# Optimization experiments

Measured on AMD Instinct MI355X. Metric: run time of the kernel, lower is better.

Reference implementation:

```python
import jax, jax.numpy as jnp
import numpy as np

NBITS = 4
GROUP_SIZE = 128


def setup_inputs() -> dict:
    key = jax.random.key(0)
    k1, k2, k3, k4, k5 = jax.random.split(key, 5)
    B, S, K, N = 2, 2048, 4096, 4096
    G = K // GROUP_SIZE  # 32 groups along K
    x = jax.random.normal(k1, (B, S, K), dtype=jnp.float16)
    # unpacked uint4 weights stored in int32 carrier, values in [0, 2^nbits)
    W_q = jax.random.randint(k2, (N, K), 0, 2 ** NBITS, dtype=jnp.int32)
    scale = (jax.random.uniform(k3, (N, G), dtype=jnp.float32) * 0.01 + 0.001).astype(jnp.float16)
    zero = (jax.random.uniform(k4, (N, G), dtype=jnp.float32) * (2 ** NBITS)).astype(jnp.float16)
    bias = jax.random.normal(k5, (N,), dtype=jnp.float16)
    return {"x": x, "W_q": W_q, "scale": scale, "zero": zero, "bias": bias}


def _dequant(W_q, scale, zero):
    # W_q: [N, K] int, scale/zero: [N, K//group_size] fp16
    # zeros_mode='original': W = (W_q - zero) * scale, per group along K
    N, K = W_q.shape
    G = K // GROUP_SIZE
    Wg = W_q.reshape(N, G, GROUP_SIZE).astype(jnp.float16)
    Wd = (Wg - zero[:, :, None]) * scale[:, :, None]
    return Wd.reshape(N, K)


def reference(x, W_q, scale, zero, bias):
    # out = x @ W_deq^T + bias   (layout 'nt': W is [N, K])
    W = _dequant(W_q, scale, zero)            # [N, K] fp16
    out = jnp.einsum('bsk,nk->bsn', x, W)     # [B, S, N] fp16 accum per module config
    return out + bias
```

## Files before the change

kernel.cpp:

```cpp
#include <hip/hip_runtime.h>
#include <hip/hip_bf16.h>


typedef __bf16 bf16x8 __attribute__((ext_vector_type(8)));
typedef float f32x4 __attribute__((ext_vector_type(4)));

#define BM 128
#define BN 128
#define BK 64

static __device__ __forceinline__ int pack_bf16x2(float a, float b) {
    __hip_bfloat162 p = __float22bfloat162_rn(make_float2(a, b));
    int r;
    __builtin_memcpy(&r, &p, 4);
    return r;
}

__global__ __launch_bounds__(256) void prepass_kernel(
    const float* __restrict__ X, unsigned short* __restrict__ Ad,
    const int*   __restrict__ Wq,
    const float* __restrict__ scale,
    const float* __restrict__ zero,
    unsigned short* __restrict__ Wd,
    int aUnits, int wUnits, int K, int G, int GROUP)
{
    const int stride = gridDim.x * blockDim.x;
    const int t0     = blockIdx.x * blockDim.x + threadIdx.x;

    for (int u = t0; u < aUnits; u += stride) {
        const long long f = (long long)u * 8;
        const float4 a0 = *(const float4*)(X + f);
        const float4 a1 = *(const float4*)(X + f + 4);
        int4 d;
        d.x = pack_bf16x2(a0.x, a0.y);
        d.y = pack_bf16x2(a0.z, a0.w);
        d.z = pack_bf16x2(a1.x, a1.y);
        d.w = pack_bf16x2(a1.z, a1.w);
        *(int4*)(Ad + f) = d;
    }

    const int unitsPerRow = K >> 3;
    for (int u = t0; u < wUnits; u += stride) {
        const int n = u / unitsPerRow;
        const int k = (u - n * unitsPerRow) * 8;
        const int g = k / GROUP;
        const float s  = scale[(long long)n * G + g];
        const float z  = zero [(long long)n * G + g];
        const float mz = -z * s;

        const long long f = (long long)n * K + k;
        const int4 q0 = *(const int4*)(Wq + f);
        const int4 q1 = *(const int4*)(Wq + f + 4);
        int4 d;
        d.x = pack_bf16x2((float)q0.x * s + mz, (float)q0.y * s + mz);
        d.y = pack_bf16x2((float)q0.z * s + mz, (float)q0.w * s + mz);
        d.z = pack_bf16x2((float)q1.x * s + mz, (float)q1.y * s + mz);
        d.w = pack_bf16x2((float)q1.z * s + mz, (float)q1.w * s + mz);
        *(int4*)(Wd + f) = d;
    }
}

__global__ __launch_bounds__(256, 2) void gemm_bf16_nt(
    const unsigned short* __restrict__ A,
    const unsigned short* __restrict__ Bw,
    const float* __restrict__ bias,
    float*       __restrict__ C,
    int M, int N, int K)
{
    __shared__ unsigned short ldsA[BM * BK];
    __shared__ unsigned short ldsB[BN * BK];

    const int tid   = threadIdx.x;
    const int lane  = tid & 63;
    const int wave  = tid >> 6;
    const int waveM = wave >> 1;
    const int waveN = wave & 1;

    const int blockN0 = blockIdx.x * BN;
    const int blockM0 = blockIdx.y * BM;

    const long long aBase = (long long)blockM0 * K;
    const long long bBase = (long long)blockN0 * K;

    const int rowInChunk = lane >> 3;
    const int colChunkSw = (lane & 7) ^ rowInChunk;
    const int col8       = colChunkSw * 8;

    f32x4 acc[4][4];
#pragma unroll
    for (int i = 0; i < 4; ++i)
#pragma unroll
        for (int j = 0; j < 4; ++j)
            acc[i][j] = (f32x4){0.f, 0.f, 0.f, 0.f};

    const int row16 = lane & 15;
    const int quad  = lane >> 4;
    const int sw    = row16 & 7;

    for (int k0 = 0; k0 < K; k0 += BK) {
        __syncthreads();
#pragma unroll
        for (int c = 0; c < 4; ++c) {
            const int chunk = (wave << 2) | c;
            const int row   = (chunk << 3) | rowInChunk;
            const unsigned short* gA = A  + aBase + (long long)row * K + k0 + col8;
            const unsigned short* gB = Bw + bBase + (long long)row * K + k0 + col8;
            __builtin_amdgcn_global_load_lds(
                (const __attribute__((address_space(1))) unsigned int*)gA,
                (__attribute__((address_space(3))) unsigned int*)&ldsA[chunk * 512],
                16, 0, 0);
            __builtin_amdgcn_global_load_lds(
                (const __attribute__((address_space(1))) unsigned int*)gB,
                (__attribute__((address_space(3))) unsigned int*)&ldsB[chunk * 512],
                16, 0, 0);
        }
        __syncthreads();

#pragma unroll
        for (int kk = 0; kk < 2; ++kk) {
            bf16x8 av[4], bv[4];
#pragma unroll
            for (int i = 0; i < 4; ++i) {
                const int r    = waveM * 64 + i * 16 + row16;
                const int slot = (kk * 4 + quad) ^ sw;
                av[i] = *(const bf16x8*)&ldsA[r * BK + slot * 8];
            }
#pragma unroll
            for (int j = 0; j < 4; ++j) {
                const int r    = waveN * 64 + j * 16 + row16;
                const int slot = (kk * 4 + quad) ^ sw;
                bv[j] = *(const bf16x8*)&ldsB[r * BK + slot * 8];
            }
#pragma unroll
            for (int i = 0; i < 4; ++i)
#pragma unroll
                for (int j = 0; j < 4; ++j)
                    acc[i][j] = __builtin_amdgcn_mfma_f32_16x16x32_bf16(
                        av[i], bv[j], acc[i][j], 0, 0, 0);
        }
    }

    const int colBase = blockN0 + waveN * 64;
    const int rowBase = blockM0 + waveM * 64;
    float biasf[4];
#pragma unroll
    for (int j = 0; j < 4; ++j)
        biasf[j] = bias[colBase + j * 16 + row16];

#pragma unroll
    for (int i = 0; i < 4; ++i) {
        const int row0 = rowBase + i * 16 + quad * 4;
#pragma unroll
        for (int j = 0; j < 4; ++j) {
            const int col = colBase + j * 16 + row16;
#pragma unroll
            for (int r = 0; r < 4; ++r) {
                C[(long long)(row0 + r) * N + col] = acc[i][j][r] + biasf[j];
            }
        }
    }
}

__global__ __launch_bounds__(256) void hqq_gemm_fused_f32(
    const float* __restrict__ A,
    const int*   __restrict__ Wq,
    const float* __restrict__ scale,
    const float* __restrict__ zero,
    const float* __restrict__ bias,
    float*       __restrict__ C,
    int M, int N, int K, int G, int GROUP)
{
    __shared__ unsigned short ldsA[BM * BK];
    __shared__ unsigned short ldsB[BN * BK];

    const int tid   = threadIdx.x;
    const int lane  = tid & 63;
    const int wave  = tid >> 6;
    const int waveM = wave >> 1;
    const int waveN = wave & 1;

    const int blockN0 = blockIdx.x * BN;
    const int blockM0 = blockIdx.y * BM;

    const int row16 = lane & 15;
    const int quad  = lane >> 4;

    f32x4 acc[4][4];
#pragma unroll
    for (int i = 0; i < 4; ++i)
#pragma unroll
        for (int j = 0; j < 4; ++j)
            acc[i][j] = (f32x4){0.f, 0.f, 0.f, 0.f};

    for (int k0 = 0; k0 < K; k0 += BK) {
        const int g = k0 / GROUP;
        int4 ra[4], rb[4];
#pragma unroll
        for (int c = 0; c < 4; ++c) {
            const int chunk = c * 256 + tid;
            const int row   = chunk >> 3;
            const int col   = (chunk & 7) * 8;

            const float* ap = A + (long long)(blockM0 + row) * K + k0 + col;
            const float4 a0 = *(const float4*)(ap);
            const float4 a1 = *(const float4*)(ap + 4);
            int4 da;
            da.x = pack_bf16x2(a0.x, a0.y);
            da.y = pack_bf16x2(a0.z, a0.w);
            da.z = pack_bf16x2(a1.x, a1.y);
            da.w = pack_bf16x2(a1.z, a1.w);
            ra[c] = da;

            const int n = blockN0 + row;
            const float s  = scale[(long long)n * G + g];
            const float z  = zero [(long long)n * G + g];
            const float mz = -z * s;
            const long long wb = (long long)n * K + k0 + col;
            const int4 q0 = *(const int4*)(Wq + wb);
            const int4 q1 = *(const int4*)(Wq + wb + 4);
            int4 db;
            db.x = pack_bf16x2((float)q0.x * s + mz, (float)q0.y * s + mz);
            db.y = pack_bf16x2((float)q0.z * s + mz, (float)q0.w * s + mz);
            db.z = pack_bf16x2((float)q1.x * s + mz, (float)q1.y * s + mz);
            db.w = pack_bf16x2((float)q1.z * s + mz, (float)q1.w * s + mz);
            rb[c] = db;
        }

        __syncthreads();
#pragma unroll
        for (int c = 0; c < 4; ++c) {
            const int chunk = c * 256 + tid;
            *(int4*)&ldsA[chunk * 8] = ra[c];
            *(int4*)&ldsB[chunk * 8] = rb[c];
        }
        __syncthreads();

#pragma unroll
        for (int kk = 0; kk < 2; ++kk) {
            const int kOff = kk * 32 + quad * 8;
            bf16x8 av[4], bv[4];
#pragma unroll
            for (int i = 0; i < 4; ++i)
                av[i] = *(const bf16x8*)&ldsA[(waveM * 64 + i * 16 + row16) * BK + kOff];
#pragma unroll
            for (int j = 0; j < 4; ++j)
                bv[j] = *(const bf16x8*)&ldsB[(waveN * 64 + j * 16 + row16) * BK + kOff];
#pragma unroll
            for (int i = 0; i < 4; ++i)
#pragma unroll
                for (int j = 0; j < 4; ++j)
                    acc[i][j] = __builtin_amdgcn_mfma_f32_16x16x32_bf16(
                        av[i], bv[j], acc[i][j], 0, 0, 0);
        }
    }

    const int colBase = blockN0 + waveN * 64;
    const int rowBase = blockM0 + waveM * 64;
    float biasf[4];
#pragma unroll
    for (int j = 0; j < 4; ++j)
        biasf[j] = bias[colBase + j * 16 + row16];

#pragma unroll
    for (int i = 0; i < 4; ++i) {
        const int row0 = rowBase + i * 16 + quad * 4;
#pragma unroll
        for (int j = 0; j < 4; ++j) {
            const int col = colBase + j * 16 + row16;
#pragma unroll
            for (int r = 0; r < 4; ++r) {
                C[(long long)(row0 + r) * N + col] = acc[i][j][r] + biasf[j];
            }
        }
    }
}

extern "C" void kernel_launch(void* const* d_in, const int* in_sizes, int n_in,
                              void* d_out, int out_size, void* d_ws, size_t ws_size,
                              hipStream_t stream) {
    (void)n_in; (void)out_size;

    const float* x     = (const float*)d_in[0];
    const int*   Wq    = (const int*)d_in[1];
    const float* scale = (const float*)d_in[2];
    const float* zero  = (const float*)d_in[3];
    const float* bias  = (const float*)d_in[4];
    float*       out   = (float*)d_out;

    const int N     = in_sizes[4];
    const int G     = in_sizes[2] / N;
    const int K     = in_sizes[1] / N;
    const int M     = in_sizes[0] / K;
    const int GROUP = K / G;

    const size_t needWs = (size_t)N * K * 2 + (size_t)M * K * 2;

    if (ws_size >= needWs) {
        unsigned short* Wd = (unsigned short*)d_ws;
        unsigned short* Ad = (unsigned short*)((char*)d_ws + (size_t)N * K * 2);

        const int aUnits = (int)((long long)M * K / 8);
        const int wUnits = (int)((long long)N * K / 8);
        prepass_kernel<<<2048, 256, 0, stream>>>(x, Ad, Wq, scale, zero, Wd,
                                                 aUnits, wUnits, K, G, GROUP);

        dim3 grid(N / BN, M / BM);
        gemm_bf16_nt<<<grid, 256, 0, stream>>>(Ad, Wd, bias, out, M, N, K);
    } else {
        dim3 grid(N / BN, M / BM);
        hqq_gemm_fused_f32<<<grid, 256, 0, stream>>>(x, Wq, scale, zero, bias, out,
                                                     M, N, K, G, GROUP);
    }
}
```

Baseline: 298.0 us.

## Add 256x256-tile bf16 GEMM with 4-deep async LDS ring and XCD swizzle

Adds a new 512-thread GEMM kernel that computes 256x256 output tiles with 8 waves. It streams A and B tiles into a 4-slot LDS ring using direct global-to-LDS loads, with a swizzled layout to avoid bank conflicts. Block IDs are remapped so neighbouring tiles land on the same XCD, and MFMA sections run at raised priority. The aim is to hide global load latency and raise operand reuse compared with the 128x128 kernel, at the cost of much more LDS and register pressure per block.

```diff
diff --git a/kernel.cpp b/kernel.cpp
--- a/kernel.cpp
+++ b/kernel.cpp
@@ -57,6 +57,161 @@
         d.z = pack_bf16x2((float)q1.x * s + mz, (float)q1.y * s + mz);
         d.w = pack_bf16x2((float)q1.z * s + mz, (float)q1.w * s + mz);
         *(int4*)(Wd + f) = d;
+    }
+}
+
+#define KT 32
+#define NRING 4
+
+__global__ __launch_bounds__(512, 2) void gemm256_bf16_nt(
+    const unsigned short* __restrict__ A,
+    const unsigned short* __restrict__ Bw,
+    const float* __restrict__ bias,
+    float*       __restrict__ C,
+    int M, int N, int K)
+{
+    __shared__ unsigned short ldsA[NRING][128 * 64];
+    __shared__ unsigned short ldsB[NRING][128 * 64];
+
+    const int tid  = threadIdx.x;
+    const int lane = tid & 63;
+    const int wave = tid >> 6;
+    const int wm   = wave >> 2;
+    const int wn   = wave & 3;
+
+    const int nwg  = (N >> 8) * (M >> 8);
+    const int cpx  = nwg >> 3;
+    const int bid  = blockIdx.x;
+    const int wgid = (bid & 7) * cpx + (bid >> 3);
+    const int bx   = wgid % (N >> 8);
+    const int by   = wgid / (N >> 8);
+    const int blockN0 = bx << 8;
+    const int blockM0 = by << 8;
+
+    long long gOffA[2], gOffB[2];
+    int ldsO[2];
+#pragma unroll
+    for (int l = 0; l < 2; ++l) {
+        const int s  = l * 512 + tid;
+        const int R  = s >> 3;
+        const int j  = s & 7;
+        const int ju = j ^ (R & 7);
+        const int r  = 2 * R + (ju >> 2);
+        const int c  = ju & 3;
+        gOffA[l] = (long long)(blockM0 + r) * K + c * 8;
+        gOffB[l] = (long long)(blockN0 + r) * K + c * 8;
+        ldsO[l]  = (l * 512 + wave * 64) * 8;
+    }
+
+    const int row16 = lane & 15;
+    const int quad  = lane >> 4;
+    int offA[8], offB[4];
+#pragma unroll
+    for (int m = 0; m < 8; ++m) {
+        const int r = wm * 128 + m * 16 + row16;
+        const int R = r >> 1;
+        const int j = ((r & 1) * 4 + quad) ^ (R & 7);
+        offA[m] = R * 64 + j * 8;
+    }
+#pragma unroll
+    for (int n = 0; n < 4; ++n) {
+        const int r = wn * 64 + n * 16 + row16;
+        const int R = r >> 1;
+        const int j = ((r & 1) * 4 + quad) ^ (R & 7);
+        offB[n] = R * 64 + j * 8;
+    }
+
+    f32x4 acc[8][4];
+#pragma unroll
+    for (int m = 0; m < 8; ++m)
+#pragma unroll
+        for (int n = 0; n < 4; ++n)
+            acc[m][n] = (f32x4){0.f, 0.f, 0.f, 0.f};
+
+#define STAGE(kt_, ring_)                                                     \
+    do {                                                                      \
+        const long long kOff_ = (long long)(kt_) * KT;                        \
+        _Pragma("unroll")                                                     \
+        for (int l = 0; l < 2; ++l) {                                         \
+            __builtin_amdgcn_global_load_lds(                                 \
+                (const __attribute__((address_space(1))) unsigned int*)       \
+                    (A + gOffA[l] + kOff_),                                   \
+                (__attribute__((address_space(3))) unsigned int*)             \
+                    (&ldsA[ring_][ldsO[l]]),                                  \
+                16, 0, 0);                                                    \
+        }                                                                     \
+        _Pragma("unroll")                                                     \
+        for (int l = 0; l < 2; ++l) {                                         \
+            __builtin_amdgcn_global_load_lds(                                 \
+                (const __attribute__((address_space(1))) unsigned int*)       \
+                    (Bw + gOffB[l] + kOff_),                                  \
+                (__attribute__((address_space(3))) unsigned int*)             \
+                    (&ldsB[ring_][ldsO[l]]),                                  \
+                16, 0, 0);                                                    \
+        }                                                                     \
+    } while (0)
+
+#define COMPUTE(ring_)                                                        \
+    do {                                                                      \
+        bf16x8 av[8], bv[4];                                                  \
+        _Pragma("unroll")                                                     \
+        for (int n = 0; n < 4; ++n)                                           \
+            bv[n] = *(const bf16x8*)&ldsB[ring_][offB[n]];                    \
+        _Pragma("unroll")                                                     \
+        for (int m = 0; m < 8; ++m)                                           \
+            av[m] = *(const bf16x8*)&ldsA[ring_][offA[m]];                    \
+        __builtin_amdgcn_s_setprio(1);                                        \
+        _Pragma("unroll")                                                     \
+        for (int m = 0; m < 8; ++m)                                           \
+            _Pragma("unroll")                                                 \
+            for (int n = 0; n < 4; ++n)                                       \
+                acc[m][n] = __builtin_amdgcn_mfma_f32_16x16x32_bf16(          \
+                    av[m], bv[n], acc[m][n], 0, 0, 0);                        \
+        __builtin_amdgcn_s_setprio(0);                                        \
+    } while (0)
+
+    const int NT = K / KT;
+
+    STAGE(0, 0);
+    STAGE(1, 1);
+    STAGE(2, 2);
+
+    for (int kt = 0; kt < NT - 3; ++kt) {
+        __builtin_amdgcn_s_barrier();
+        STAGE(kt + 3, (kt + 3) & 3);
+        asm volatile("s_waitcnt vmcnt(8)" ::: "memory");
+        __builtin_amdgcn_s_barrier();
+        COMPUTE(kt & 3);
+    }
+
+    __builtin_amdgcn_s_barrier();
+    asm volatile("s_waitcnt vmcnt(0)" ::: "memory");
+    __builtin_amdgcn_s_barrier();
+    COMPUTE((NT - 3) & 3);
+    COMPUTE((NT - 2) & 3);
+    COMPUTE((NT - 1) & 3);
+
+#undef STAGE
+#undef COMPUTE
+
+    const int colBase = blockN0 + wn * 64;
+    const int rowBase = blockM0 + wm * 128;
+    float biasf[4];
+#pragma unroll
+    for (int n = 0; n < 4; ++n)
+        biasf[n] = bias[colBase + n * 16 + row16];
+
+#pragma unroll
+    for (int m = 0; m < 8; ++m) {
+        const int row0 = rowBase + m * 16 + quad * 4;
+#pragma unroll
+        for (int n = 0; n < 4; ++n) {
+            const int col = colBase + n * 16 + row16;
+#pragma unroll
+            for (int r = 0; r < 4; ++r) {
+                C[(long long)(row0 + r) * N + col] = acc[m][n][r] + biasf[n];
+            }
+        }
     }
 }
 
@@ -304,8 +459,13 @@
         prepass_kernel<<<2048, 256, 0, stream>>>(x, Ad, Wq, scale, zero, Wd,
                                                  aUnits, wUnits, K, G, GROUP);
 
-        dim3 grid(N / BN, M / BM);
-        gemm_bf16_nt<<<grid, 256, 0, stream>>>(Ad, Wd, bias, out, M, N, K);
+        const int nwg = (N >> 8) * (M >> 8);
+        if ((M % 256) == 0 && (N % 256) == 0 && (K % 128) == 0 && (nwg % 8) == 0) {
+            gemm256_bf16_nt<<<nwg, 512, 0, stream>>>(Ad, Wd, bias, out, M, N, K);
+        } else {
+            dim3 grid(N / BN, M / BM);
+            gemm_bf16_nt<<<grid, 256, 0, stream>>>(Ad, Wd, bias, out, M, N, K);
+        }
     } else {
         dim3 grid(N / BN, M / BM);
         hqq_gemm_fused_f32<<<grid, 256, 0, stream>>>(x, Wq, scale, zero, bias, out,
```

New measurement: 321.7 us. 1.08x slower.
